# Kernel tuning notes

Measured on AMD Instinct MI355X. Metric: run time of the kernel, lower is better.

Reference implementation:

```python
import jax, jax.numpy as jnp
import numpy as np

B, T, D, U = 64, 1024, 300, 300


def setup_inputs() -> dict:
    key = jax.random.key(0)
    ks = jax.random.split(key, 12)
    inputs = jax.random.normal(ks[0], (B, T, D), jnp.float32)
    lengths = jax.random.randint(ks[1], (B,), T // 2, T + 1)
    mask = jnp.arange(T)[None, :] < lengths[:, None]  # [B,T] bool

    def w(k, shape, fan_in):
        return jax.random.normal(k, shape, jnp.float32) * (1.0 / np.sqrt(fan_in))

    # Keras GRU (reset_after=True): kernel [D,3U], recurrent_kernel [U,3U], bias [2,3U]
    k_fwd = w(ks[2], (D, 3 * U), D)
    rk_fwd = w(ks[3], (U, 3 * U), U)
    b_fwd = jnp.zeros((2, 3 * U), jnp.float32)
    k_bwd = w(ks[4], (D, 3 * U), D)
    rk_bwd = w(ks[5], (U, 3 * U), U)
    b_bwd = jnp.zeros((2, 3 * U), jnp.float32)
    w_fc = w(ks[6], (2 * U, U), 2 * U)
    b_fc = jnp.zeros((U,), jnp.float32)
    return {
        "inputs": inputs, "mask": mask,
        "k_fwd": k_fwd, "rk_fwd": rk_fwd, "b_fwd": b_fwd,
        "k_bwd": k_bwd, "rk_bwd": rk_bwd, "b_bwd": b_bwd,
        "w_fc": w_fc, "b_fc": b_fc, "training": 0,
    }


def _gru_dir(x, mask, kernel, rkernel, bias):
    """Keras GRU v2 (reset_after=True), zero_output_for_mask, state frozen on masked steps.
    x: [B,T,D], mask: [B,T] bool -> (ys [B,T,U], h_final [B,U])"""
    b_in, b_rec = bias[0], bias[1]
    u = rkernel.shape[0]
    # precompute input projections for all timesteps (cuDNN-style hoisting)
    xp = jnp.einsum('btd,dk->btk', x, kernel) + b_in  # [B,T,3U]

    def step(h, inp):
        xt, mt = inp  # xt: [B,3U], mt: [B]
        rp = h @ rkernel + b_rec  # [B,3U]
        xz, xr, xh = jnp.split(xt, 3, axis=-1)
        rz, rr, rh = jnp.split(rp, 3, axis=-1)
        z = jax.nn.sigmoid(xz + rz)
        r = jax.nn.sigmoid(xr + rr)
        hh = jnp.tanh(xh + r * rh)
        h_new = z * h + (1.0 - z) * hh
        m = mt[:, None]
        h_carry = jnp.where(m, h_new, h)       # state does not update on masked steps
        y = jnp.where(m, h_new, jnp.zeros_like(h_new))  # zero_output_for_mask
        return h_carry, y

    h0 = jnp.zeros((x.shape[0], u), x.dtype)
    h_final, ys = jax.lax.scan(step, h0, (xp.transpose(1, 0, 2), mask.T))
    return ys.transpose(1, 0, 2), h_final


def reference(inputs, mask, k_fwd, rk_fwd, b_fwd, k_bwd, rk_bwd, b_bwd, w_fc, b_fc, training):
    mask = mask.astype(bool)
    x = inputs  # Dropout is identity at inference (training=0)
    y_f, h_f = _gru_dir(x, mask, k_fwd, rk_fwd, b_fwd)
    # backward direction: process reversed sequence/mask, then re-reverse outputs
    y_b, h_b = _gru_dir(x[:, ::-1], mask[:, ::-1], k_bwd, rk_bwd, b_bwd)
    y_b = y_b[:, ::-1]
    output = jnp.concatenate([y_f, y_b], axis=-1)  # [B,T,2U]
    state = jax.nn.relu(jnp.concatenate([h_f, h_b], axis=-1) @ w_fc + b_fc)  # [B,U]
    return output, state
```

## Files before the change

### kernel.cpp

```cpp
#include <hip/hip_runtime.h>
#include <hip/hip_bf16.h>


#define B_   64
#define T_   1024
#define D_   300
#define U_   300
#define NU   900
#define KP   320
#define NP   960
#define XPW  912
#define KB_  10
#define KRES 2
#define HSP  328
#define FRAGS_PER_DIR 570
#define NRESF 114
#define NWGM 4

typedef short short8 __attribute__((ext_vector_type(8)));
typedef float floatx4 __attribute__((ext_vector_type(4)));

__device__ __forceinline__ float b2f_bits(unsigned short u) {
  union { unsigned int i; float f; } v; v.i = ((unsigned int)u) << 16; return v.f;
}
__device__ __forceinline__ unsigned short f2b(float f) {
  __hip_bfloat16 h = __float2bfloat16(f);
  return *reinterpret_cast<unsigned short*>(&h);
}
__device__ __forceinline__ float sigm_f(float x) {
  float e = __expf(-x);
  return __fdividef(1.f, 1.f + e);
}
__device__ __forceinline__ float tanh_f(float x) {
  float e = __expf(2.f * x);
  return 1.f - __fdividef(2.f, e + 1.f);
}

__global__ __launch_bounds__(64) void k_detect(const unsigned int* __restrict__ xw,
                                               const unsigned char* __restrict__ mb,
                                               int* __restrict__ flags) {
  __shared__ int red[64];
  int tid = threadIdx.x;
  int hits = 0;
  for (int i = tid; i < 2048; i += 64) {
    unsigned int lo = xw[i] & 0xFFFFu;
    int e = (int)((lo >> 7) & 0xFF);
    if (e >= 105 && e <= 135) hits++;
  }
  red[tid] = hits;
  __syncthreads();
  if (tid == 0) {
    int s = 0;
    for (int i = 0; i < 64; ++i) s += red[i];
    flags[0] = (s >= 1024) ? 1 : 0;
    unsigned char b0 = mb[0], b1 = mb[1];
    flags[1] = (b1 == 0) ? 0 : ((b0 == 1 && b1 == 1) ? 1 : 2);
  }
}

__global__ __launch_bounds__(256) void k_lengths(const unsigned char* __restrict__ mraw,
                                                 const int* __restrict__ flags,
                                                 int* __restrict__ lens) {
  __shared__ int red[256];
  int b = blockIdx.x, tid = threadIdx.x;
  int mt = flags[1];
  int s = 0;
  if (mt == 0) {
    const int* m = (const int*)mraw;
    for (int t = tid; t < T_; t += 256) s += m[(size_t)b * T_ + t] ? 1 : 0;
  } else if (mt == 1) {
    for (int t = tid; t < T_; t += 256) s += mraw[(size_t)b * T_ + t] ? 1 : 0;
  } else {
    const unsigned short* m = (const unsigned short*)mraw;
    for (int t = tid; t < T_; t += 256) s += m[(size_t)b * T_ + t] ? 1 : 0;
  }
  red[tid] = s; __syncthreads();
  for (int off = 128; off > 0; off >>= 1) {
    if (tid < off) red[tid] += red[tid + off];
    __syncthreads();
  }
  if (tid == 0) lens[b] = red[0];
}

__global__ __launch_bounds__(256) void k_xpad(const void* __restrict__ xraw,
                                              const int* __restrict__ flags,
                                              unsigned short* __restrict__ xp) {
  int id = blockIdx.x * 256 + threadIdx.x;
  int row = id / 40, seg = id % 40;
  int kbase = seg * 8;
  int bf = flags[0];
  unsigned short v[8];
  if (bf) {
    const unsigned short* x = (const unsigned short*)xraw;
#pragma unroll
    for (int i = 0; i < 8; ++i) {
      int k = kbase + i;
      v[i] = (k < D_) ? x[(size_t)row * D_ + k] : (unsigned short)0;
    }
  } else {
    const float* x = (const float*)xraw;
#pragma unroll
    for (int i = 0; i < 8; ++i) {
      int k = kbase + i;
      v[i] = (k < D_) ? f2b(x[(size_t)row * D_ + k]) : (unsigned short)0;
    }
  }
  uint4 o;
  o.x = (unsigned)v[0] | ((unsigned)v[1] << 16);
  o.y = (unsigned)v[2] | ((unsigned)v[3] << 16);
  o.z = (unsigned)v[4] | ((unsigned)v[5] << 16);
  o.w = (unsigned)v[6] | ((unsigned)v[7] << 16);
  *(uint4*)(xp + (size_t)row * KP + kbase) = o;
}

__global__ __launch_bounds__(256) void k_wpad(const void* __restrict__ kf,
                                              const void* __restrict__ kb,
                                              const int* __restrict__ flags,
                                              unsigned short* __restrict__ kp) {
  int id = blockIdx.x * 256 + threadIdx.x;
  if (id >= 2 * KP * NP) return;
  int dir = id / (KP * NP);
  int r = id % (KP * NP);
  int k = r / NP, n = r % NP;
  int bf = flags[0];
  unsigned short v = 0;
  if (k < D_ && n < NU) {
    size_t si = (size_t)k * NU + n;
    if (bf) v = ((const unsigned short*)(dir ? kb : kf))[si];
    else    v = f2b(((const float*)(dir ? kb : kf))[si]);
  }
  kp[id] = v;
}

__global__ __launch_bounds__(256) void k_prep(const void* __restrict__ rkf,
                                              const void* __restrict__ rkb,
                                              const void* __restrict__ bfw,
                                              const void* __restrict__ bbw,
                                              const void* __restrict__ wfc,
                                              const void* __restrict__ bfc,
                                              const int* __restrict__ flags,
                                              unsigned short* __restrict__ rkc,
                                              float* __restrict__ biasc,
                                              unsigned short* __restrict__ wfcc,
                                              float* __restrict__ bfcc) {
  int i = blockIdx.x * 256 + threadIdx.x;
  int bf = flags[0];
  if (i < 2 * D_ * NU) {
    int dir = i / (D_ * NU), r = i % (D_ * NU);
    const void* src = dir ? rkb : rkf;
    rkc[i] = bf ? ((const unsigned short*)src)[r] : f2b(((const float*)src)[r]);
  }
  if (i < 2 * 2 * NU) {
    int dir = i / (2 * NU), r = i % (2 * NU);
    const void* src = dir ? bbw : bfw;
    biasc[i] = bf ? b2f_bits(((const unsigned short*)src)[r]) : ((const float*)src)[r];
  }
  if (i < 2 * U_ * U_) {
    wfcc[i] = bf ? ((const unsigned short*)wfc)[i] : f2b(((const float*)wfc)[i]);
  }
  if (i < U_) {
    bfcc[i] = bf ? b2f_bits(((const unsigned short*)bfc)[i]) : ((const float*)bfc)[i];
  }
}

__global__ __launch_bounds__(256) void k_bpack(const unsigned short* __restrict__ rkc,
                                               unsigned short* __restrict__ bpack) {
  int idx = blockIdx.x * 256 + threadIdx.x;
  const int total = 2 * FRAGS_PER_DIR * 512;
  if (idx >= total) return;
  int rem = idx;
  int j = rem & 7; rem >>= 3;
  int lane = rem & 63; rem >>= 6;
  int f = rem % FRAGS_PER_DIR;
  int dir = rem / FRAGS_PER_DIR;
  int w, fr, ntc;
  if (f < 270) { w = f / 90; fr = f - w * 90; ntc = 9; }
  else { int f2 = f - 270; w = 3 + f2 / 60; fr = f2 % 60; ntc = 6; }
  int kb = fr / ntc, nt = fr % ntc;
  int lb = nt / 3, g = nt % 3;
  int ub0 = (w < 3) ? w * 3 : 9 + (w - 3) * 2;
  int l15 = lane & 15, quad = lane >> 4;
  int k = kb * 32 + quad * 8 + j;
  int u = (ub0 + lb) * 16 + l15;
  unsigned short v = 0;
  if (k < U_ && u < U_) {
    v = rkc[(size_t)dir * U_ * NU + (size_t)k * NU + (size_t)g * U_ + u];
  }
  bpack[idx] = v;
}

template <bool XPF32>
__global__ __launch_bounds__(256) void k_gemm(const unsigned short* __restrict__ xpad,
                                              const unsigned short* __restrict__ kpad,
                                              const float* __restrict__ biasc,
                                              void* __restrict__ xp_out) {
  __shared__ __align__(16) unsigned short As[64 * 40];
  __shared__ __align__(16) unsigned short Bs[64 * 40];
  int tid = threadIdx.x;
  int wave = tid >> 6, lane = tid & 63;
  int m0 = blockIdx.x * 64, n0 = blockIdx.y * 64;
  int dir = blockIdx.z;
  const unsigned short* Bsrc = kpad + (size_t)dir * KP * NP;
  const float* bin = biasc + (size_t)dir * 2 * NU;

  floatx4 acc[4];
#pragma unroll
  for (int i = 0; i < 4; ++i) acc[i] = {0.f, 0.f, 0.f, 0.f};

  int arow = tid >> 2, aseg = tid & 3;
  int bk = tid & 31, bn8 = (tid >> 5) * 8;
  int fr = lane & 15, fq = lane >> 4;

  for (int kc = 0; kc < KP; kc += 32) {
    uint4 av = *(const uint4*)(xpad + (size_t)(m0 + arow) * KP + kc + aseg * 8);
    uint4 bv = *(const uint4*)(Bsrc + (size_t)(kc + bk) * NP + n0 + bn8);
    *(uint4*)(As + arow * 40 + aseg * 8) = av;
    unsigned short tmp[8];
    tmp[0] = bv.x & 0xffff; tmp[1] = bv.x >> 16;
    tmp[2] = bv.y & 0xffff; tmp[3] = bv.y >> 16;
    tmp[4] = bv.z & 0xffff; tmp[5] = bv.z >> 16;
    tmp[6] = bv.w & 0xffff; tmp[7] = bv.w >> 16;
#pragma unroll
    for (int i = 0; i < 8; ++i) Bs[(bn8 + i) * 40 + bk] = tmp[i];
    __syncthreads();
    short8 a = *(const short8*)(As + (wave * 16 + fr) * 40 + fq * 8);
#pragma unroll
    for (int nt = 0; nt < 4; ++nt) {
      short8 bfrag = *(const short8*)(Bs + (nt * 16 + fr) * 40 + fq * 8);
      acc[nt] = __builtin_amdgcn_mfma_f32_16x16x32_bf16(a, bfrag, acc[nt], 0, 0, 0);
    }
    __syncthreads();
  }
#pragma unroll
  for (int nt = 0; nt < 4; ++nt) {
    int col = n0 + nt * 16 + fr;
    if (col >= XPW) continue;
    float bi = (col < NU) ? bin[col] : 0.f;
#pragma unroll
    for (int r = 0; r < 4; ++r) {
      int m = m0 + wave * 16 + fq * 4 + r;
      float v = acc[nt][r] + bi;
      size_t idx = ((size_t)dir * 65536 + m) * XPW + col;
      if (XPF32) ((float*)xp_out)[idx] = v;
      else ((unsigned short*)xp_out)[idx] = f2b(v);
    }
  }
}

template <int NTC, int D, bool XPF32>
__device__ __forceinline__ void scan_loop(
    const unsigned short* __restrict__ bp,
    const unsigned short* __restrict__ sBw,
    unsigned short (*sHiP)[16][HSP],
    unsigned short (*sLoP)[16][HSP],
    const void* __restrict__ xp_all,
    unsigned short* __restrict__ out16, float* __restrict__ out32, int obf,
    const float* __restrict__ brec, const int* __restrict__ lens,
    float* __restrict__ hfin,
    int dir, int mg, int ub0, int l15, int quad) {
  constexpr int NB = NTC / 3;
  constexpr int NSTR = KB_ - KRES;

  int ucl[NB]; bool cv[NB];
  float bz[NB], brg[NB], bh[NB];
#pragma unroll
  for (int lb = 0; lb < NB; ++lb) {
    int u = (ub0 + lb) * 16 + l15;
    bool v = (u < U_);
    cv[lb] = v;
    ucl[lb] = v ? u : 0;
    bz[lb] = brec[ucl[lb]]; brg[lb] = brec[U_ + ucl[lb]]; bh[lb] = brec[2 * U_ + ucl[lb]];
  }
  size_t xbase[4];
#pragma unroll
  for (int r = 0; r < 4; ++r)
    xbase[r] = ((size_t)dir * 65536 + (size_t)(mg * 16 + quad * 4 + r) * T_) * XPW;
  int mylen[4];
#pragma unroll
  for (int r = 0; r < 4; ++r) mylen[r] = lens[mg * 16 + quad * 4 + r];
  float hold[NB][4];
#pragma unroll
  for (int lb = 0; lb < NB; ++lb)
#pragma unroll
    for (int r = 0; r < 4; ++r) hold[lb][r] = 0.f;

#pragma unroll 1
  for (int s = 0; s < T_; ++s) {
    const int t = dir ? (T_ - 1 - s) : s;
    const int par = s & 1;
    const unsigned short (*hH)[HSP] = sHiP[par];
    const unsigned short (*hL)[HSP] = sLoP[par];

    floatx4 acc[NTC];
#pragma unroll
    for (int i = 0; i < NTC; ++i) acc[i] = {0.f, 0.f, 0.f, 0.f};

    short8 buf[D][NTC];
#pragma unroll
    for (int d = 0; d < D; ++d)
#pragma unroll
      for (int nt = 0; nt < NTC; ++nt)
        buf[d][nt] = *(const short8*)(bp + ((size_t)((KRES + d) * NTC + nt)) * 512);

    float X[NB][3][4];
#pragma unroll
    for (int r = 0; r < 4; ++r) {
      size_t ro = xbase[r] + (size_t)t * XPW;
      if (XPF32) {
        const float* xr = (const float*)xp_all + ro;
#pragma unroll
        for (int lb = 0; lb < NB; ++lb) {
          X[lb][0][r] = xr[ucl[lb]];
          X[lb][1][r] = xr[U_ + ucl[lb]];
          X[lb][2][r] = xr[2 * U_ + ucl[lb]];
        }
      } else {
        const unsigned short* xr = (const unsigned short*)xp_all + ro;
#pragma unroll
        for (int lb = 0; lb < NB; ++lb) {
          X[lb][0][r] = b2f_bits(xr[ucl[lb]]);
          X[lb][1][r] = b2f_bits(xr[U_ + ucl[lb]]);
          X[lb][2][r] = b2f_bits(xr[2 * U_ + ucl[lb]]);
        }
      }
    }

#pragma unroll
    for (int kb = 0; kb < KRES; ++kb) {
      short8 ah = *(const short8*)&hH[l15][kb * 32 + quad * 8];
      short8 al = *(const short8*)&hL[l15][kb * 32 + quad * 8];
#pragma unroll
      for (int nt = 0; nt < NTC; ++nt) {
        short8 b = *(const short8*)(sBw + ((size_t)(kb * NTC + nt)) * 512);
        acc[nt] = __builtin_amdgcn_mfma_f32_16x16x32_bf16(ah, b, acc[nt], 0, 0, 0);
      }
#pragma unroll
      for (int nt = 0; nt < NTC; ++nt) {
        short8 b = *(const short8*)(sBw + ((size_t)(kb * NTC + nt)) * 512);
        acc[nt] = __builtin_amdgcn_mfma_f32_16x16x32_bf16(al, b, acc[nt], 0, 0, 0);
      }
    }

#pragma unroll
    for (int i = 0; i < NSTR; ++i) {
      const int kb = KRES + i;
      short8 ah = *(const short8*)&hH[l15][kb * 32 + quad * 8];
      short8 al = *(const short8*)&hL[l15][kb * 32 + quad * 8];
#pragma unroll
      for (int nt = 0; nt < NTC; ++nt)
        acc[nt] = __builtin_amdgcn_mfma_f32_16x16x32_bf16(ah, buf[i % D][nt], acc[nt], 0, 0, 0);
#pragma unroll
      for (int nt = 0; nt < NTC; ++nt)
        acc[nt] = __builtin_amdgcn_mfma_f32_16x16x32_bf16(al, buf[i % D][nt], acc[nt], 0, 0, 0);
      if (i + D < NSTR) {
#pragma unroll
        for (int nt = 0; nt < NTC; ++nt)
          buf[i % D][nt] = *(const short8*)(bp + ((size_t)((kb + D) * NTC + nt)) * 512);
      }
    }

    unsigned short (*nHi)[HSP] = sHiP[par ^ 1];
    unsigned short (*nLo)[HSP] = sLoP[par ^ 1];
#pragma unroll
    for (int r = 0; r < 4; ++r) {
      const int row = quad * 4 + r;
      const bool m = (t < mylen[r]);
      const size_t ob = ((size_t)(mg * 16 + row) * T_ + t) * 600 + (size_t)dir * U_;
#pragma unroll
      for (int lb = 0; lb < NB; ++lb) {
        float z  = sigm_f(X[lb][0][r] + acc[lb * 3 + 0][r] + bz[lb]);
        float rg = sigm_f(X[lb][1][r] + acc[lb * 3 + 1][r] + brg[lb]);
        float hh = tanh_f(X[lb][2][r] + rg * (acc[lb * 3 + 2][r] + bh[lb]));
        float hn = z * hold[lb][r] + (1.f - z) * hh;
        float hw = m ? hn : hold[lb][r];
        hold[lb][r] = hw;
        if (cv[lb]) {
          float y = m ? hn : 0.f;
          if (obf) out16[ob + ucl[lb]] = f2b(y); else out32[ob + ucl[lb]] = y;
          unsigned short hib = f2b(hw);
          nHi[row][ucl[lb]] = hib;
          nLo[row][ucl[lb]] = f2b(hw - b2f_bits(hib));
        }
      }
    }

    asm volatile("s_waitcnt lgkmcnt(0)" ::: "memory");
    __builtin_amdgcn_s_barrier();
  }

#pragma unroll
  for (int lb = 0; lb < NB; ++lb) {
    if (!cv[lb]) continue;
#pragma unroll
    for (int r = 0; r < 4; ++r)
      hfin[((size_t)dir * B_ + mg * 16 + quad * 4 + r) * 304 + ucl[lb]] = hold[lb][r];
  }
}

template <bool XPF32>
__global__ __launch_bounds__(512, 2) void k_scan(const unsigned short* __restrict__ bpack,
                                                 const float* __restrict__ biasc,
                                                 const void* __restrict__ xp_all,
                                                 const int* __restrict__ lens,
                                                 const int* __restrict__ flags,
                                                 float* __restrict__ hfin,
                                                 void* __restrict__ outraw) {
  __shared__ unsigned short sHi[2][16][HSP];
  __shared__ unsigned short sLo[2][16][HSP];
  __shared__ __align__(16) unsigned short sB[NRESF * 512];

  const int tid = threadIdx.x;
  const int mg = blockIdx.x;
  const int dir = blockIdx.y;
  const int wave = tid >> 6, lane = tid & 63;
  const int l15 = lane & 15, quad = lane >> 4;
  const int obf = flags[0];
  unsigned short* out16 = (unsigned short*)outraw;
  float* out32 = (float*)outraw;

  const int NTCw = (wave < 3) ? 9 : 6;
  const int UB0w = (wave < 3) ? wave * 3 : 9 + (wave - 3) * 2;
  const int FB   = (wave < 3) ? wave * 90 : 270 + (wave - 3) * 60;
  const int RB   = (wave < 3) ? wave * 18 : 54 + (wave - 3) * 12;

  {
    unsigned int* p0 = (unsigned int*)&sHi[0][0][0];
    unsigned int* p1 = (unsigned int*)&sLo[0][0][0];
    for (int i = tid; i < 2 * 16 * HSP / 2; i += 512) { p0[i] = 0u; p1[i] = 0u; }
  }
  {
    const unsigned short* src = bpack + ((size_t)dir * FRAGS_PER_DIR + FB) * 512 + lane * 8;
    unsigned short* dst = sB + (size_t)RB * 512 + lane * 8;
    for (int j = 0; j < KRES * NTCw; ++j)
      *(uint4*)(dst + (size_t)j * 512) = *(const uint4*)(src + (size_t)j * 512);
  }
  __syncthreads();

  const unsigned short* bp = bpack + ((size_t)dir * FRAGS_PER_DIR + FB) * 512 + (size_t)lane * 8;
  const unsigned short* sBw = sB + (size_t)RB * 512 + (size_t)lane * 8;
  const float* brec = biasc + (size_t)dir * 2 * NU + NU;

  if (wave < 3)
    scan_loop<9, 3, XPF32>(bp, sBw, sHi, sLo, xp_all, out16, out32, obf, brec, lens,
                           hfin, dir, mg, UB0w, l15, quad);
  else
    scan_loop<6, 4, XPF32>(bp, sBw, sHi, sLo, xp_all, out16, out32, obf, brec, lens,
                           hfin, dir, mg, UB0w, l15, quad);
}

__global__ __launch_bounds__(320) void k_state(const float* __restrict__ hfin,
                                               const unsigned short* __restrict__ wfcc,
                                               const float* __restrict__ bfcc,
                                               const int* __restrict__ flags,
                                               void* __restrict__ outraw) {
  int b = blockIdx.x, u = threadIdx.x;
  if (u >= U_) return;
  int obf = flags[0];
  float acc = bfcc[u];
  const float* hf = hfin + (size_t)b * 304;
  const float* hb = hfin + ((size_t)B_ + b) * 304;
  for (int k = 0; k < U_; ++k) acc = fmaf(hf[k], b2f_bits(wfcc[(size_t)k * U_ + u]), acc);
  for (int k = 0; k < U_; ++k) acc = fmaf(hb[k], b2f_bits(wfcc[(size_t)(U_ + k) * U_ + u]), acc);
  float v = fmaxf(acc, 0.f);
  size_t oi = (size_t)B_ * T_ * 600 + (size_t)b * U_ + u;
  if (obf) ((unsigned short*)outraw)[oi] = f2b(v);
  else     ((float*)outraw)[oi] = v;
}

extern "C" void kernel_launch(void* const* d_in, const int* in_sizes, int n_in,
                              void* d_out, int out_size, void* d_ws, size_t ws_size,
                              hipStream_t stream) {
  const void* x    = d_in[0];
  const void* mask = d_in[1];
  const void* kf   = d_in[2];
  const void* rkf  = d_in[3];
  const void* bfw  = d_in[4];
  const void* kb   = d_in[5];
  const void* rkb  = d_in[6];
  const void* bbw  = d_in[7];
  const void* wfc  = d_in[8];
  const void* bfc  = d_in[9];

  char* ws = (char*)d_ws;
  size_t off = 0;
  auto alloc = [&](size_t bytes) { void* p = ws + off; off += (bytes + 255) & ~(size_t)255; return p; };
  int* flags            = (int*)alloc(256);
  int* lens             = (int*)alloc(256);
  unsigned short* xpad  = (unsigned short*)alloc((size_t)65536 * KP * 2);
  unsigned short* kpad  = (unsigned short*)alloc((size_t)2 * KP * NP * 2);
  unsigned short* rkc   = (unsigned short*)alloc((size_t)2 * D_ * NU * 2);
  unsigned short* bpack = (unsigned short*)alloc((size_t)2 * FRAGS_PER_DIR * 512 * 2);
  float* biasc          = (float*)alloc((size_t)2 * 2 * NU * 4);
  unsigned short* wfcc  = (unsigned short*)alloc((size_t)2 * U_ * U_ * 2);
  float* bfcc           = (float*)alloc((size_t)U_ * 4);
  float* hfin           = (float*)alloc((size_t)2 * B_ * 304 * 4);
  void* xp = (void*)(ws + off);
  size_t need_f32 = off + (size_t)2 * 65536 * XPW * 4;
  bool xpf32 = ws_size >= need_f32;

  k_detect<<<dim3(1), dim3(64), 0, stream>>>((const unsigned int*)x, (const unsigned char*)mask, flags);
  k_lengths<<<dim3(B_), dim3(256), 0, stream>>>((const unsigned char*)mask, flags, lens);
  k_xpad<<<dim3(65536 * 40 / 256), dim3(256), 0, stream>>>(x, flags, xpad);
  k_wpad<<<dim3((2 * KP * NP + 255) / 256), dim3(256), 0, stream>>>(kf, kb, flags, kpad);
  k_prep<<<dim3((2 * D_ * NU + 255) / 256), dim3(256), 0, stream>>>(rkf, rkb, bfw, bbw, wfc, bfc,
                                                                    flags, rkc, biasc, wfcc, bfcc);
  k_bpack<<<dim3((2 * FRAGS_PER_DIR * 512 + 255) / 256), dim3(256), 0, stream>>>(rkc, bpack);
  if (xpf32) {
    k_gemm<true><<<dim3(1024, 15, 2), dim3(256), 0, stream>>>(xpad, kpad, biasc, xp);
    k_scan<true><<<dim3(NWGM, 2), dim3(512), 0, stream>>>(bpack, biasc, xp, lens, flags, hfin, d_out);
  } else {
    k_gemm<false><<<dim3(1024, 15, 2), dim3(256), 0, stream>>>(xpad, kpad, biasc, xp);
    k_scan<false><<<dim3(NWGM, 2), dim3(512), 0, stream>>>(bpack, biasc, xp, lens, flags, hfin, d_out);
  }
  k_state<<<dim3(B_), dim3(320), 0, stream>>>(hfin, wfcc, bfcc, flags, d_out);
}
```

Before: 14.69 ms.

## Stream recurrent weights via async global-to-LDS DMA double buffer in scan

Replaces the per-step register-prefetched global weight loads (with two K-blocks resident in LDS) with a two-slot LDS window filled by global_load_lds DMA, one K-block ahead. The K-block order alternates forward and backward between steps so the blocks still in the window can be reused. It also prefetches the next timestep's input projections into a second register set while the gates are computed, hiding that latency. This relieves register pressure and overlaps weight streaming with MFMA, at the cost of more vmcnt/lgkmcnt waits, and it relies on each wave's DMA completing before it reads its own slot.

```diff
diff --git a/kernel.cpp b/kernel.cpp
--- a/kernel.cpp
+++ b/kernel.cpp
@@ -11,14 +11,16 @@
 #define NP   960
 #define XPW  912
 #define KB_  10
-#define KRES 2
 #define HSP  328
 #define FRAGS_PER_DIR 570
-#define NRESF 114
+#define SLOTF 57
+#define SLOTSH (SLOTF*512)
 #define NWGM 4
 
 typedef short short8 __attribute__((ext_vector_type(8)));
 typedef float floatx4 __attribute__((ext_vector_type(4)));
+
+template <bool V> struct BoolC { static constexpr bool value = V; };
 
 __device__ __forceinline__ float b2f_bits(unsigned short u) {
   union { unsigned int i; float f; } v; v.i = ((unsigned int)u) << 16; return v.f;
@@ -34,6 +36,17 @@
 __device__ __forceinline__ float tanh_f(float x) {
   float e = __expf(2.f * x);
   return 1.f - __fdividef(2.f, e + 1.f);
+}
+__device__ __forceinline__ void wait_lgkm0() {
+  asm volatile("s_waitcnt lgkmcnt(0)" ::: "memory");
+}
+template <int N> __device__ __forceinline__ void wait_vm() {
+  asm volatile("s_waitcnt vmcnt(%0)" :: "n"(N) : "memory");
+}
+__device__ __forceinline__ void dma16(const unsigned short* g, unsigned short* l) {
+  __builtin_amdgcn_global_load_lds(
+      (const __attribute__((address_space(1))) unsigned int*)g,
+      (__attribute__((address_space(3))) unsigned int*)l, 16, 0, 0);
 }
 
 __global__ __launch_bounds__(64) void k_detect(const unsigned int* __restrict__ xw,
@@ -247,19 +260,18 @@
   }
 }
 
-template <int NTC, int D, bool XPF32>
+template <int NTC, bool XPF32>
 __device__ __forceinline__ void scan_loop(
-    const unsigned short* __restrict__ bp,
-    const unsigned short* __restrict__ sBw,
+    const unsigned short* __restrict__ bpL,
+    unsigned short* __restrict__ winw,
     unsigned short (*sHiP)[16][HSP],
     unsigned short (*sLoP)[16][HSP],
     const void* __restrict__ xp_all,
     unsigned short* __restrict__ out16, float* __restrict__ out32, int obf,
     const float* __restrict__ brec, const int* __restrict__ lens,
     float* __restrict__ hfin,
-    int dir, int mg, int ub0, int l15, int quad) {
+    int dir, int mg, int ub0, int l15, int quad, int lane) {
   constexpr int NB = NTC / 3;
-  constexpr int NSTR = KB_ - KRES;
 
   int ucl[NB]; bool cv[NB];
   float bz[NB], brg[NB], bh[NB];
@@ -272,42 +284,28 @@
     bz[lb] = brec[ucl[lb]]; brg[lb] = brec[U_ + ucl[lb]]; bh[lb] = brec[2 * U_ + ucl[lb]];
   }
   size_t xbase[4];
-#pragma unroll
-  for (int r = 0; r < 4; ++r)
+  int mylen[4];
+#pragma unroll
+  for (int r = 0; r < 4; ++r) {
     xbase[r] = ((size_t)dir * 65536 + (size_t)(mg * 16 + quad * 4 + r) * T_) * XPW;
-  int mylen[4];
-#pragma unroll
-  for (int r = 0; r < 4; ++r) mylen[r] = lens[mg * 16 + quad * 4 + r];
+    mylen[r] = lens[mg * 16 + quad * 4 + r];
+  }
   float hold[NB][4];
 #pragma unroll
   for (int lb = 0; lb < NB; ++lb)
 #pragma unroll
     for (int r = 0; r < 4; ++r) hold[lb][r] = 0.f;
 
-#pragma unroll 1
-  for (int s = 0; s < T_; ++s) {
-    const int t = dir ? (T_ - 1 - s) : s;
-    const int par = s & 1;
-    const unsigned short (*hH)[HSP] = sHiP[par];
-    const unsigned short (*hL)[HSP] = sLoP[par];
-
-    floatx4 acc[NTC];
-#pragma unroll
-    for (int i = 0; i < NTC; ++i) acc[i] = {0.f, 0.f, 0.f, 0.f};
-
-    short8 buf[D][NTC];
-#pragma unroll
-    for (int d = 0; d < D; ++d)
-#pragma unroll
-      for (int nt = 0; nt < NTC; ++nt)
-        buf[d][nt] = *(const short8*)(bp + ((size_t)((KRES + d) * NTC + nt)) * 512);
-
-    float X[NB][3][4];
+  const unsigned short* winL = winw + (size_t)lane * 8;
+
+  unsigned int XA[NB][3][4], XB[NB][3][4];
+
+  auto load_xp = [&](unsigned int (&X)[NB][3][4], int t) {
 #pragma unroll
     for (int r = 0; r < 4; ++r) {
       size_t ro = xbase[r] + (size_t)t * XPW;
       if (XPF32) {
-        const float* xr = (const float*)xp_all + ro;
+        const unsigned int* xr = (const unsigned int*)xp_all + ro;
 #pragma unroll
         for (int lb = 0; lb < NB; ++lb) {
           X[lb][0][r] = xr[ucl[lb]];
@@ -318,49 +316,71 @@
         const unsigned short* xr = (const unsigned short*)xp_all + ro;
 #pragma unroll
         for (int lb = 0; lb < NB; ++lb) {
-          X[lb][0][r] = b2f_bits(xr[ucl[lb]]);
-          X[lb][1][r] = b2f_bits(xr[U_ + ucl[lb]]);
-          X[lb][2][r] = b2f_bits(xr[2 * U_ + ucl[lb]]);
+          X[lb][0][r] = (unsigned int)xr[ucl[lb]];
+          X[lb][1][r] = (unsigned int)xr[U_ + ucl[lb]];
+          X[lb][2][r] = (unsigned int)xr[2 * U_ + ucl[lb]];
         }
       }
     }
-
-#pragma unroll
-    for (int kb = 0; kb < KRES; ++kb) {
+  };
+  auto xval = [&](unsigned int x) -> float {
+    if (XPF32) { union { unsigned int i; float f; } v; v.i = x; return v.f; }
+    return b2f_bits((unsigned short)x);
+  };
+  auto dma_kb = [&](int kb) {
+    const unsigned short* g = bpL + (size_t)kb * NTC * 512;
+    unsigned short* l = winw + (size_t)(kb & 1) * SLOTSH;
+#pragma unroll
+    for (int nt = 0; nt < NTC; ++nt)
+      dma16(g + (size_t)nt * 512, l + (size_t)nt * 512);
+  };
+
+  dma_kb(0);
+  dma_kb(1);
+  load_xp(XA, dir ? (T_ - 1) : 0);
+  asm volatile("s_waitcnt vmcnt(0)" ::: "memory");
+  __syncthreads();
+
+  auto step = [&](auto fwd_c, int s, unsigned int (&Xu)[NB][3][4],
+                  unsigned int (&Xp)[NB][3][4]) {
+    constexpr bool FWD = decltype(fwd_c)::value;
+    const int t = dir ? (T_ - 1 - s) : s;
+    const int par = s & 1;
+    const unsigned short (*hH)[HSP] = sHiP[par];
+    const unsigned short (*hL)[HSP] = sLoP[par];
+
+    floatx4 acc[NTC];
+#pragma unroll
+    for (int i = 0; i < NTC; ++i) acc[i] = {0.f, 0.f, 0.f, 0.f};
+
+#pragma unroll
+    for (int i = 0; i < 10; ++i) {
+      const int kb = FWD ? i : 9 - i;
+      if (i >= 2 && i <= 8) wait_vm<NTC>();
+      if (i == 9) wait_vm<0>();
       short8 ah = *(const short8*)&hH[l15][kb * 32 + quad * 8];
       short8 al = *(const short8*)&hL[l15][kb * 32 + quad * 8];
-#pragma unroll
-      for (int nt = 0; nt < NTC; ++nt) {
-        short8 b = *(const short8*)(sBw + ((size_t)(kb * NTC + nt)) * 512);
-        acc[nt] = __builtin_amdgcn_mfma_f32_16x16x32_bf16(ah, b, acc[nt], 0, 0, 0);
-      }
-#pragma unroll
-      for (int nt = 0; nt < NTC; ++nt) {
-        short8 b = *(const short8*)(sBw + ((size_t)(kb * NTC + nt)) * 512);
-        acc[nt] = __builtin_amdgcn_mfma_f32_16x16x32_bf16(al, b, acc[nt], 0, 0, 0);
-      }
-    }
-
-#pragma unroll
-    for (int i = 0; i < NSTR; ++i) {
-      const int kb = KRES + i;
-      short8 ah = *(const short8*)&hH[l15][kb * 32 + quad * 8];
-      short8 al = *(const short8*)&hL[l15][kb * 32 + quad * 8];
+      short8 bfr[NTC];
 #pragma unroll
       for (int nt = 0; nt < NTC; ++nt)
-        acc[nt] = __builtin_amdgcn_mfma_f32_16x16x32_bf16(ah, buf[i % D][nt], acc[nt], 0, 0, 0);
+        bfr[nt] = *(const short8*)(winL + (size_t)(kb & 1) * SLOTSH + (size_t)nt * 512);
 #pragma unroll
       for (int nt = 0; nt < NTC; ++nt)
-        acc[nt] = __builtin_amdgcn_mfma_f32_16x16x32_bf16(al, buf[i % D][nt], acc[nt], 0, 0, 0);
-      if (i + D < NSTR) {
-#pragma unroll
-        for (int nt = 0; nt < NTC; ++nt)
-          buf[i % D][nt] = *(const short8*)(bp + ((size_t)((kb + D) * NTC + nt)) * 512);
-      }
-    }
-
-    unsigned short (*nHi)[HSP] = sHiP[par ^ 1];
-    unsigned short (*nLo)[HSP] = sLoP[par ^ 1];
+        acc[nt] = __builtin_amdgcn_mfma_f32_16x16x32_bf16(ah, bfr[nt], acc[nt], 0, 0, 0);
+#pragma unroll
+      for (int nt = 0; nt < NTC; ++nt)
+        acc[nt] = __builtin_amdgcn_mfma_f32_16x16x32_bf16(al, bfr[nt], acc[nt], 0, 0, 0);
+      wait_lgkm0();
+      if (i <= 7) dma_kb(FWD ? i + 2 : 7 - i);
+    }
+
+    {
+      int tn = dir ? (t > 0 ? t - 1 : t) : (t < T_ - 1 ? t + 1 : t);
+      load_xp(Xp, tn);
+    }
+
+    unsigned short (*nH)[HSP] = sHiP[par ^ 1];
+    unsigned short (*nL)[HSP] = sLoP[par ^ 1];
 #pragma unroll
     for (int r = 0; r < 4; ++r) {
       const int row = quad * 4 + r;
@@ -368,9 +388,9 @@
       const size_t ob = ((size_t)(mg * 16 + row) * T_ + t) * 600 + (size_t)dir * U_;
 #pragma unroll
       for (int lb = 0; lb < NB; ++lb) {
-        float z  = sigm_f(X[lb][0][r] + acc[lb * 3 + 0][r] + bz[lb]);
-        float rg = sigm_f(X[lb][1][r] + acc[lb * 3 + 1][r] + brg[lb]);
-        float hh = tanh_f(X[lb][2][r] + rg * (acc[lb * 3 + 2][r] + bh[lb]));
+        float z  = sigm_f(xval(Xu[lb][0][r]) + acc[lb * 3 + 0][r] + bz[lb]);
+        float rg = sigm_f(xval(Xu[lb][1][r]) + acc[lb * 3 + 1][r] + brg[lb]);
+        float hh = tanh_f(xval(Xu[lb][2][r]) + rg * (acc[lb * 3 + 2][r] + bh[lb]));
         float hn = z * hold[lb][r] + (1.f - z) * hh;
         float hw = m ? hn : hold[lb][r];
         hold[lb][r] = hw;
@@ -378,14 +398,19 @@
           float y = m ? hn : 0.f;
           if (obf) out16[ob + ucl[lb]] = f2b(y); else out32[ob + ucl[lb]] = y;
           unsigned short hib = f2b(hw);
-          nHi[row][ucl[lb]] = hib;
-          nLo[row][ucl[lb]] = f2b(hw - b2f_bits(hib));
+          nH[row][ucl[lb]] = hib;
+          nL[row][ucl[lb]] = f2b(hw - b2f_bits(hib));
         }
       }
     }
-
-    asm volatile("s_waitcnt lgkmcnt(0)" ::: "memory");
+    wait_lgkm0();
     __builtin_amdgcn_s_barrier();
+  };
+
+#pragma unroll 1
+  for (int s = 0; s < T_; s += 2) {
+    step(BoolC<true>{}, s, XA, XB);
+    step(BoolC<false>{}, s + 1, XB, XA);
   }
 
 #pragma unroll
@@ -407,7 +432,7 @@
                                                  void* __restrict__ outraw) {
   __shared__ unsigned short sHi[2][16][HSP];
   __shared__ unsigned short sLo[2][16][HSP];
-  __shared__ __align__(16) unsigned short sB[NRESF * 512];
+  __shared__ __align__(16) unsigned short win[2 * SLOTSH];
 
   const int tid = threadIdx.x;
   const int mg = blockIdx.x;
@@ -418,34 +443,26 @@
   unsigned short* out16 = (unsigned short*)outraw;
   float* out32 = (float*)outraw;
 
-  const int NTCw = (wave < 3) ? 9 : 6;
   const int UB0w = (wave < 3) ? wave * 3 : 9 + (wave - 3) * 2;
   const int FB   = (wave < 3) ? wave * 90 : 270 + (wave - 3) * 60;
-  const int RB   = (wave < 3) ? wave * 18 : 54 + (wave - 3) * 12;
+  const int RBW  = (wave < 3) ? wave * 9 : 27 + (wave - 3) * 6;
 
   {
     unsigned int* p0 = (unsigned int*)&sHi[0][0][0];
     unsigned int* p1 = (unsigned int*)&sLo[0][0][0];
     for (int i = tid; i < 2 * 16 * HSP / 2; i += 512) { p0[i] = 0u; p1[i] = 0u; }
   }
-  {
-    const unsigned short* src = bpack + ((size_t)dir * FRAGS_PER_DIR + FB) * 512 + lane * 8;
-    unsigned short* dst = sB + (size_t)RB * 512 + lane * 8;
-    for (int j = 0; j < KRES * NTCw; ++j)
-      *(uint4*)(dst + (size_t)j * 512) = *(const uint4*)(src + (size_t)j * 512);
-  }
-  __syncthreads();
-
-  const unsigned short* bp = bpack + ((size_t)dir * FRAGS_PER_DIR + FB) * 512 + (size_t)lane * 8;
-  const unsigned short* sBw = sB + (size_t)RB * 512 + (size_t)lane * 8;
+
+  const unsigned short* bpL = bpack + ((size_t)dir * FRAGS_PER_DIR + FB) * 512 + (size_t)lane * 8;
+  unsigned short* winw = &win[(size_t)RBW * 512];
   const float* brec = biasc + (size_t)dir * 2 * NU + NU;
 
   if (wave < 3)
-    scan_loop<9, 3, XPF32>(bp, sBw, sHi, sLo, xp_all, out16, out32, obf, brec, lens,
-                           hfin, dir, mg, UB0w, l15, quad);
+    scan_loop<9, XPF32>(bpL, winw, sHi, sLo, xp_all, out16, out32, obf, brec, lens,
+                        hfin, dir, mg, UB0w, l15, quad, lane);
   else
-    scan_loop<6, 4, XPF32>(bp, sBw, sHi, sLo, xp_all, out16, out32, obf, brec, lens,
-                           hfin, dir, mg, UB0w, l15, quad);
+    scan_loop<6, XPF32>(bpL, winw, sHi, sLo, xp_all, out16, out32, obf, brec, lens,
+                        hfin, dir, mg, UB0w, l15, quad, lane);
 }
 
 __global__ __launch_bounds__(320) void k_state(const float* __restrict__ hfin,
```

Result: no change. 14.59 ms (-0.7%).
